# Performance work log

Measured on AMD Instinct MI355X. Metric: run time of the kernel, lower is better.

Reference implementation:

```python
import jax, jax.numpy as jnp
import numpy as np

N_NODES = 100000
N_EDGES = 3200000
IN_FEATS = 128
HIDDEN = 64
N_CLASSES = 16


def gcn_conv(x, src, dst, W, b, num_nodes):
    """PyG GCNConv (default settings): add self-loops, symmetric norm,
    linear transform, scatter-sum aggregation at dst, then bias."""
    # degree counts include self-loops (fill value 1.0)
    deg = jnp.zeros((num_nodes,), x.dtype).at[dst].add(1.0) + 1.0
    dinv = jax.lax.rsqrt(deg)  # deg >= 1, no inf handling needed
    h = x @ W  # [N, out]
    # edge messages: norm(src,dst) * h[src], aggregated at dst
    norm = dinv[src] * dinv[dst]  # [E]
    msg = h[src] * norm[:, None]  # [E, out]
    out = jax.ops.segment_sum(msg, dst, num_segments=num_nodes)
    # self-loop contribution: norm = dinv[i]^2
    out = out + h * (dinv * dinv)[:, None]
    return out + b


def setup_inputs() -> dict:
    key = jax.random.key(0)
    k1, k2, k3, k4 = jax.random.split(key, 4)
    x = jax.random.normal(k1, (N_NODES, IN_FEATS), dtype=jnp.float32)
    edge_index = jax.random.randint(k2, (2, N_EDGES), 0, N_NODES, dtype=jnp.int64)
    W1 = jax.random.normal(k3, (IN_FEATS, HIDDEN), dtype=jnp.float32) * (1.0 / np.sqrt(IN_FEATS))
    b1 = jnp.zeros((HIDDEN,), jnp.float32)
    W2 = jax.random.normal(k4, (HIDDEN, N_CLASSES), dtype=jnp.float32) * (1.0 / np.sqrt(HIDDEN))
    b2 = jnp.zeros((N_CLASSES,), jnp.float32)
    return {"x": x, "edge_index": edge_index, "W1": W1, "b1": b1, "W2": W2, "b2": b2}


def reference(x, edge_index, W1, b1, W2, b2):
    src, dst = edge_index[0], edge_index[1]
    h = gcn_conv(x, src, dst, W1, b1, N_NODES)
    h = jax.nn.relu(h)  # dropout is identity in eval mode
    out = gcn_conv(h, src, dst, W2, b2, N_NODES)
    return out
```

## Files before the change

### kernel.cpp

```cpp
#include <hip/hip_runtime.h>
#include <hip/hip_fp16.h>
#include <stdint.h>

#define N_NODES   100000
#define N_HALF    50000
#define N_EDGES   3200000
#define F_IN      128
#define F_HID     64
#define F_OUT     16

typedef _Float16 h2v __attribute__((ext_vector_type(2)));
typedef _Float16 h4v __attribute__((ext_vector_type(4)));
typedef _Float16 h8v __attribute__((ext_vector_type(8)));
typedef float    f4v __attribute__((ext_vector_type(4)));

#define BSHIFT    7
#define BK        128
#define NBUCK     782
#define NBLK_P    800
#define CHUNK_E   (N_EDGES / NBLK_P)
#define PSTRIDE   4992

#define G1_TM     64
#define G1_BLOCKS ((N_NODES + G1_TM - 1) / G1_TM)

#define OFF_RS       0
#define OFF_LEN      400000
#define OFF_DINV     800000
#define OFF_GCNT     1200000
#define OFF_CSR      1203200
#define OFF_HS1      9010688
#define OFF_OUT1A    21810688
#define OFF_OUT1B    34610688
#define OFF_HS2      47410688
#define OFF_PAIRS    OFF_OUT1A

__global__ __launch_bounds__(256, 4) void k_partition(const void* __restrict__ ei,
                                                      int* __restrict__ gcnt,
                                                      unsigned* __restrict__ pairs) {
    __shared__ unsigned long long st[CHUNK_E];
    __shared__ int h[NBUCK];
    __shared__ int cur[NBUCK];
    __shared__ int is64s;
    int t = threadIdx.x;
    if (t < 64) {
        const unsigned* u = (const unsigned*)ei;
        unsigned lo = u[2 * t], hi = u[2 * t + 1];
        int bad = (hi != 0u || lo >= 100000u) ? 1 : 0;
        unsigned long long mask = __ballot(bad);
        if (t == 0) is64s = (mask == 0ull);
    }
    for (int i = t; i < NBUCK; i += 256) { h[i] = 0; }
    __syncthreads();
    int shift = 2 + is64s;
    const char* sp = (const char*)ei;
    const char* dp = sp + ((size_t)N_EDGES << shift);
#define LDS_IDX(p, e) __builtin_nontemporal_load((const unsigned*)((p) + ((size_t)(e) << shift)))
    int base = blockIdx.x * CHUNK_E;
    int i = t;
    for (; i + 768 < CHUNK_E; i += 1024) {
        int e0 = base + i, e1 = e0 + 256, e2 = e0 + 512, e3 = e0 + 768;
        unsigned s0 = LDS_IDX(sp, e0), s1 = LDS_IDX(sp, e1);
        unsigned s2 = LDS_IDX(sp, e2), s3 = LDS_IDX(sp, e3);
        unsigned d0 = LDS_IDX(dp, e0), d1 = LDS_IDX(dp, e1);
        unsigned d2 = LDS_IDX(dp, e2), d3 = LDS_IDX(dp, e3);
        st[i]       = ((unsigned long long)s0 << 32) | d0;
        st[i + 256] = ((unsigned long long)s1 << 32) | d1;
        st[i + 512] = ((unsigned long long)s2 << 32) | d2;
        st[i + 768] = ((unsigned long long)s3 << 32) | d3;
        atomicAdd(&h[d0 >> BSHIFT], 1);
        atomicAdd(&h[d1 >> BSHIFT], 1);
        atomicAdd(&h[d2 >> BSHIFT], 1);
        atomicAdd(&h[d3 >> BSHIFT], 1);
    }
    for (; i < CHUNK_E; i += 256) {
        unsigned s = LDS_IDX(sp, base + i);
        unsigned d = LDS_IDX(dp, base + i);
        st[i] = ((unsigned long long)s << 32) | d;
        atomicAdd(&h[d >> BSHIFT], 1);
    }
#undef LDS_IDX
    __syncthreads();
    for (int j = t; j < NBUCK; j += 256) {
        int c = h[j];
        cur[j] = c ? atomicAdd(&gcnt[j], c) : 0;
    }
    __syncthreads();
    i = t;
    for (; i + 768 < CHUNK_E; i += 1024) {
        unsigned long long v0 = st[i],       v1 = st[i + 256];
        unsigned long long v2 = st[i + 512], v3 = st[i + 768];
        unsigned d0 = (unsigned)v0, d1 = (unsigned)v1;
        unsigned d2 = (unsigned)v2, d3 = (unsigned)v3;
        int p0 = atomicAdd(&cur[d0 >> BSHIFT], 1);
        int p1 = atomicAdd(&cur[d1 >> BSHIFT], 1);
        int p2 = atomicAdd(&cur[d2 >> BSHIFT], 1);
        int p3 = atomicAdd(&cur[d3 >> BSHIFT], 1);
        if (p0 < PSTRIDE) pairs[(d0 >> BSHIFT) * PSTRIDE + p0] = ((unsigned)(v0 >> 32) << BSHIFT) | (d0 & (BK - 1u));
        if (p1 < PSTRIDE) pairs[(d1 >> BSHIFT) * PSTRIDE + p1] = ((unsigned)(v1 >> 32) << BSHIFT) | (d1 & (BK - 1u));
        if (p2 < PSTRIDE) pairs[(d2 >> BSHIFT) * PSTRIDE + p2] = ((unsigned)(v2 >> 32) << BSHIFT) | (d2 & (BK - 1u));
        if (p3 < PSTRIDE) pairs[(d3 >> BSHIFT) * PSTRIDE + p3] = ((unsigned)(v3 >> 32) << BSHIFT) | (d3 & (BK - 1u));
    }
    for (; i < CHUNK_E; i += 256) {
        unsigned long long v = st[i];
        unsigned d = (unsigned)v;
        int b = d >> BSHIFT;
        int p = atomicAdd(&cur[b], 1);
        if (p < PSTRIDE)
            pairs[b * PSTRIDE + p] = ((unsigned)(v >> 32) << BSHIFT) | (d & (BK - 1u));
    }
}

__global__ __launch_bounds__(512) void k_build(const unsigned* __restrict__ pairs,
                                               const int* __restrict__ gcnt,
                                               int* __restrict__ rowstart,
                                               int* __restrict__ lens,
                                               float* __restrict__ dinv,
                                               unsigned short* __restrict__ csr) {
    __shared__ unsigned prS[PSTRIDE];
    __shared__ unsigned short csrS[PSTRIDE];
    __shared__ int c0S[BK], c1S[BK], scanS[BK], pos0[BK], pos1[BK];
    __shared__ int totpadS;
    int b = blockIdx.x, t = threadIdx.x;
    if (t < BK) { c0S[t] = 0; c1S[t] = 0; }
    __syncthreads();
    int tot = gcnt[b]; if (tot > PSTRIDE) tot = PSTRIDE;
    int base = b * PSTRIDE;
    for (int i = t; i < tot; i += 512) {
        unsigned pr = __builtin_nontemporal_load(pairs + base + i);
        prS[i] = pr;
        if ((pr >> BSHIFT) < (unsigned)N_HALF) atomicAdd(&c0S[pr & (BK - 1u)], 1);
        else                                   atomicAdd(&c1S[pr & (BK - 1u)], 1);
    }
    __syncthreads();
    int tpad = 0, p0a = 0;
    if (t < BK) {
        p0a = (c0S[t] + 3) & ~3;
        tpad = p0a + ((c1S[t] + 3) & ~3);
        scanS[t] = tpad;
    }
    __syncthreads();
    for (int off = 1; off < BK; off <<= 1) {
        int add = 0;
        if (t < BK && t >= off) add = scanS[t - off];
        __syncthreads();
        if (t < BK) scanS[t] += add;
        __syncthreads();
    }
    if (t < BK) {
        int rs = scanS[t] - tpad;
        pos0[t] = rs;
        pos1[t] = rs + p0a;
        int d = (b << BSHIFT) + t;
        if (d < N_NODES) {
            rowstart[d] = base + rs;
            lens[d] = c0S[t] | (c1S[t] << 16);
            dinv[d] = rsqrtf((float)(c0S[t] + c1S[t]) + 1.0f);
        }
        if (t == BK - 1) totpadS = scanS[BK - 1];
    }
    __syncthreads();
    for (int i = t; i < tot; i += 512) {
        unsigned pr = prS[i];
        unsigned s = pr >> BSHIFT;
        int d = pr & (BK - 1u);
        if (s < (unsigned)N_HALF) {
            int p = atomicAdd(&pos0[d], 1);
            csrS[p] = (unsigned short)s;
        } else {
            int p = atomicAdd(&pos1[d], 1);
            csrS[p] = (unsigned short)(s - N_HALF);
        }
    }
    __syncthreads();
    int nchunk = (totpadS + 7) >> 3;
    uint4* dst = (uint4*)(csr + base);
    const uint4* srcp = (const uint4*)csrS;
    for (int i = t; i < nchunk; i += 512) dst[i] = srcp[i];
}

__global__ __launch_bounds__(256, 4) void k_gemm1(const float* __restrict__ x,
                                                  const float* __restrict__ W1,
                                                  const float* __restrict__ dinv,
                                                  __half* __restrict__ hs1) {
    __shared__ _Float16 W1s[F_IN * F_HID];
    int t = threadIdx.x;
    for (int idx = t; idx < F_IN * F_HID; idx += 256) {
        int k = idx >> 6, n = idx & 63;
        float v = W1[idx];
        int kc = k >> 5, ko = (k >> 3) & 3, j = k & 7;
        int nt = n >> 4, c = n & 15;
        W1s[((kc * 4 + ko) * 4 + nt) * 128 + c * 8 + j] = (_Float16)v;
    }
    __syncthreads();
    int w = t >> 6, l = t & 63;
    int lm = l & 15, lk = l >> 4;
    int nblock = blockIdx.x * G1_TM;
    int anode = nblock + w * 16 + lm;
    int anodec = anode < N_NODES ? anode : N_NODES - 1;
    f4v acc[4] = {};
    const h8v* Bp = (const h8v*)W1s;
#pragma unroll
    for (int kc = 0; kc < 4; ++kc) {
        const f4v* src = (const f4v*)(x + (size_t)anodec * F_IN + kc * 32 + lk * 8);
        f4v v0 = __builtin_nontemporal_load(src);
        f4v v1 = __builtin_nontemporal_load(src + 1);
        h8v a;
#pragma unroll
        for (int i = 0; i < 4; ++i) {
            a[i]     = (_Float16)v0[i];
            a[i + 4] = (_Float16)v1[i];
        }
#pragma unroll
        for (int nt = 0; nt < 4; ++nt) {
            h8v b = Bp[((kc * 4 + lk) * 4 + nt) * 16 + lm];
            acc[nt] = __builtin_amdgcn_mfma_f32_16x16x32_f16(a, b, acc[nt], 0, 0, 0);
        }
    }
#pragma unroll
    for (int r = 0; r < 4; ++r) {
        int node = nblock + w * 16 + lk * 4 + r;
        if (node < N_NODES) {
            float dv = dinv[node];
#pragma unroll
            for (int nt = 0; nt < 4; ++nt) {
                float val = acc[nt][r] * dv;
                hs1[((size_t)(nt >> 1) * N_NODES + node) * 32 + (nt & 1) * 16 + lm] =
                    __float2half(val);
            }
        }
    }
}

__global__ __launch_bounds__(256) void k_agg1(const __half* __restrict__ hs1,
                                              const unsigned short* __restrict__ csr,
                                              const int* __restrict__ rowstart,
                                              const int* __restrict__ lens,
                                              __half* __restrict__ out1a,
                                              __half* __restrict__ out1b) {
    int bid = blockIdx.x;
    int combo = bid & 3;
    int chunk = combo & 1, half = combo >> 1;
    int nb = bid >> 2;
    int w = threadIdx.x >> 6, lane = threadIdx.x & 63;
    int slot = lane >> 3, fp = lane & 7;
    int n = nb * 32 + w * 8 + slot;
    const char* T = (const char*)hs1
                  + (size_t)chunk * ((size_t)N_NODES * 64)
                  + (size_t)half * ((size_t)N_HALF * 64);
    unsigned fo = fp * 8u;
    int rs = rowstart[n];
    int L = lens[n];
    int c0 = L & 0xffff;
    int start = half ? (rs + ((c0 + 3) & ~3)) : rs;
    int c = half ? (L >> 16) : c0;
    h4v a0 = {(_Float16)0.f, (_Float16)0.f, (_Float16)0.f, (_Float16)0.f};
    h4v a1 = a0, a2 = a0, a3 = a0;
    const unsigned long long* Q = (const unsigned long long*)csr;
    int q0 = start >> 2;
    int nq = c >> 2;
#define ROW1(idx) (*(const h4v*)(T + (unsigned)(idx) * 64u + fo))
    int q = 0;
    unsigned long long ea = 0ull, eb = 0ull;
    if (q + 2 <= nq) { ea = Q[q0]; eb = Q[q0 + 1]; }
    while (q + 2 <= nq) {
        unsigned long long ca = ea, cb = eb;
        q += 2;
        if (q + 2 <= nq) { ea = Q[q0 + q]; eb = Q[q0 + q + 1]; }
        h4v t0 = ROW1(ca & 0xffffu);
        h4v t1 = ROW1((ca >> 16) & 0xffffu);
        h4v t2 = ROW1((ca >> 32) & 0xffffu);
        h4v t3 = ROW1(ca >> 48);
        h4v t4 = ROW1(cb & 0xffffu);
        h4v t5 = ROW1((cb >> 16) & 0xffffu);
        h4v t6 = ROW1((cb >> 32) & 0xffffu);
        h4v t7 = ROW1(cb >> 48);
        a0 += t0; a1 += t1; a2 += t2; a3 += t3;
        a0 += t4; a1 += t5; a2 += t6; a3 += t7;
    }
    if (q < nq) {
        unsigned long long e = Q[q0 + q];
        a0 += ROW1(e & 0xffffu);
        a1 += ROW1((e >> 16) & 0xffffu);
        a2 += ROW1((e >> 32) & 0xffffu);
        a3 += ROW1(e >> 48);
    }
    for (int j = start + (nq << 2); j < start + c; ++j)
        a0 += ROW1(csr[j]);
    if ((n >= N_HALF) == (half != 0))
        a1 += ROW1(n - half * N_HALF);
#undef ROW1
    float s0 = ((float)a0[0] + (float)a1[0]) + ((float)a2[0] + (float)a3[0]);
    float s1 = ((float)a0[1] + (float)a1[1]) + ((float)a2[1] + (float)a3[1]);
    float s2 = ((float)a0[2] + (float)a1[2]) + ((float)a2[2] + (float)a3[2]);
    float s3 = ((float)a0[3] + (float)a1[3]) + ((float)a2[3] + (float)a3[3]);
    union { __half2 h[2]; float2 f; } u;
    u.h[0] = __floats2half2_rn(s0, s1);
    u.h[1] = __floats2half2_rn(s2, s3);
    __half* dst = (half ? out1b : out1a) + (size_t)n * F_HID + chunk * 32 + fp * 4;
    *(float2*)dst = u.f;
}

__global__ __launch_bounds__(256) void k_gemm2(const __half* __restrict__ out1a,
                                               const __half* __restrict__ out1b,
                                               const float* __restrict__ W2,
                                               const float* __restrict__ dinv,
                                               const float* __restrict__ b1,
                                               __half* __restrict__ hs2) {
    __shared__ float ws[F_HID * F_OUT];
    __shared__ float b1s[F_HID];
    int t = threadIdx.x;
    ((float4*)ws)[t] = ((const float4*)W2)[t];
    if (t < 16) ((float4*)b1s)[t] = ((const float4*)b1)[t];
    __syncthreads();
    int tid = blockIdx.x * 256 + t;
    int n = tid >> 2;
    if (n >= N_NODES) return;
    int cq = (tid & 3) << 2;
    float dv = dinv[n];
    const h2v* A = (const h2v*)(out1a + (size_t)n * F_HID);
    const h2v* B = (const h2v*)(out1b + (size_t)n * F_HID);
    float4 acc = make_float4(0.f, 0.f, 0.f, 0.f);
#pragma unroll 4
    for (int k4 = 0; k4 < 16; ++k4) {
        h2v pa0 = A[k4 * 2], pa1 = A[k4 * 2 + 1];
        h2v pb0 = B[k4 * 2], pb1 = B[k4 * 2 + 1];
        float h0 = fmaxf(dv * ((float)pa0.x + (float)pb0.x) + b1s[k4 * 4 + 0], 0.f);
        float h1 = fmaxf(dv * ((float)pa0.y + (float)pb0.y) + b1s[k4 * 4 + 1], 0.f);
        float h2 = fmaxf(dv * ((float)pa1.x + (float)pb1.x) + b1s[k4 * 4 + 2], 0.f);
        float h3 = fmaxf(dv * ((float)pa1.y + (float)pb1.y) + b1s[k4 * 4 + 3], 0.f);
        float4 w0 = *(const float4*)(ws + (k4 * 4 + 0) * F_OUT + cq);
        float4 w1 = *(const float4*)(ws + (k4 * 4 + 1) * F_OUT + cq);
        float4 w2 = *(const float4*)(ws + (k4 * 4 + 2) * F_OUT + cq);
        float4 w3 = *(const float4*)(ws + (k4 * 4 + 3) * F_OUT + cq);
        acc.x += h0 * w0.x + h1 * w1.x + h2 * w2.x + h3 * w3.x;
        acc.y += h0 * w0.y + h1 * w1.y + h2 * w2.y + h3 * w3.y;
        acc.z += h0 * w0.z + h1 * w1.z + h2 * w2.z + h3 * w3.z;
        acc.w += h0 * w0.w + h1 * w1.w + h2 * w2.w + h3 * w3.w;
    }
    union { __half2 h2x[2]; float2 f; } u;
    u.h2x[0] = __floats2half2_rn(acc.x * dv, acc.y * dv);
    u.h2x[1] = __floats2half2_rn(acc.z * dv, acc.w * dv);
    *(float2*)(hs2 + (size_t)n * F_OUT + cq) = u.f;
}

__global__ __launch_bounds__(128) void k_agg2(const __half* __restrict__ hs2,
                                              const unsigned short* __restrict__ csr,
                                              const int* __restrict__ rowstart,
                                              const int* __restrict__ lens,
                                              const float* __restrict__ dinv,
                                              const float* __restrict__ b2,
                                              float* __restrict__ out) {
    int w = threadIdx.x >> 6, lane = threadIdx.x & 63;
    int slot = lane >> 2, fp = lane & 3;
    int n = blockIdx.x * 32 + w * 16 + slot;
    unsigned fo = fp * 8u;
    int rs = rowstart[n];
    int L = lens[n];
    int c0 = L & 0xffff, c1 = L >> 16;
    const unsigned long long* Q = (const unsigned long long*)csr;
    h4v a0 = {(_Float16)0.f, (_Float16)0.f, (_Float16)0.f, (_Float16)0.f};
    h4v a1 = a0, a2 = a0, a3 = a0;
#pragma unroll
    for (int half = 0; half < 2; ++half) {
        const char* T = (const char*)hs2 + (size_t)half * ((size_t)N_HALF * 32);
        int start = half ? (rs + ((c0 + 3) & ~3)) : rs;
        int c = half ? c1 : c0;
        int q0 = start >> 2;
        int nq = c >> 2;
#define ROW2(idx) (*(const h4v*)(T + (unsigned)(idx) * 32u + fo))
        int q = 0;
        unsigned long long ea = 0ull, eb = 0ull;
        if (q + 2 <= nq) { ea = Q[q0]; eb = Q[q0 + 1]; }
        while (q + 2 <= nq) {
            unsigned long long ca = ea, cb = eb;
            q += 2;
            if (q + 2 <= nq) { ea = Q[q0 + q]; eb = Q[q0 + q + 1]; }
            h4v t0 = ROW2(ca & 0xffffu);
            h4v t1 = ROW2((ca >> 16) & 0xffffu);
            h4v t2 = ROW2((ca >> 32) & 0xffffu);
            h4v t3 = ROW2(ca >> 48);
            h4v t4 = ROW2(cb & 0xffffu);
            h4v t5 = ROW2((cb >> 16) & 0xffffu);
            h4v t6 = ROW2((cb >> 32) & 0xffffu);
            h4v t7 = ROW2(cb >> 48);
            a0 += t0; a1 += t1; a2 += t2; a3 += t3;
            a0 += t4; a1 += t5; a2 += t6; a3 += t7;
        }
        if (q < nq) {
            unsigned long long e = Q[q0 + q];
            a0 += ROW2(e & 0xffffu);
            a1 += ROW2((e >> 16) & 0xffffu);
            a2 += ROW2((e >> 32) & 0xffffu);
            a3 += ROW2(e >> 48);
        }
        for (int j = start + (nq << 2); j < start + c; ++j)
            a0 += ROW2(csr[j]);
#undef ROW2
    }
    a1 += *(const h4v*)((const char*)hs2 + (unsigned)n * 32u + fo);
    float dv = dinv[n];
    int fb = fp * 4;
    float s0 = ((float)a0[0] + (float)a1[0]) + ((float)a2[0] + (float)a3[0]);
    float s1 = ((float)a0[1] + (float)a1[1]) + ((float)a2[1] + (float)a3[1]);
    float s2 = ((float)a0[2] + (float)a1[2]) + ((float)a2[2] + (float)a3[2]);
    float s3 = ((float)a0[3] + (float)a1[3]) + ((float)a2[3] + (float)a3[3]);
    float ox0 = dv * s0 + b2[fb + 0];
    float ox1 = dv * s1 + b2[fb + 1];
    float ox2 = dv * s2 + b2[fb + 2];
    float ox3 = dv * s3 + b2[fb + 3];
    float4* dst = (float4*)(out + (size_t)n * F_OUT + fb);
    *dst = make_float4(ox0, ox1, ox2, ox3);
}

extern "C" void kernel_launch(void* const* d_in, const int* in_sizes, int n_in,
                              void* d_out, int out_size, void* d_ws, size_t ws_size,
                              hipStream_t stream) {
    const float* x  = (const float*)d_in[0];
    const void*  ei = d_in[1];
    const float* W1 = (const float*)d_in[2];
    const float* b1 = (const float*)d_in[3];
    const float* W2 = (const float*)d_in[4];
    const float* b2 = (const float*)d_in[5];
    float* out = (float*)d_out;

    char* ws = (char*)d_ws;
    int*            rowstart = (int*)(ws + OFF_RS);
    int*            lens     = (int*)(ws + OFF_LEN);
    float*          dinv     = (float*)(ws + OFF_DINV);
    int*            gcnt     = (int*)(ws + OFF_GCNT);
    unsigned short* csr      = (unsigned short*)(ws + OFF_CSR);
    __half*         hs1      = (__half*)(ws + OFF_HS1);
    __half*         out1a    = (__half*)(ws + OFF_OUT1A);
    __half*         out1b    = (__half*)(ws + OFF_OUT1B);
    __half*         hs2      = (__half*)(ws + OFF_HS2);
    unsigned*       pairs    = (unsigned*)(ws + OFF_PAIRS);

    (void)hipMemsetAsync(gcnt, 0, NBUCK * sizeof(int), stream);
    k_partition<<<NBLK_P, 256, 0, stream>>>(ei, gcnt, pairs);
    k_build    <<<NBUCK, 512, 0, stream>>>(pairs, gcnt, rowstart, lens, dinv, csr);

    k_gemm1<<<G1_BLOCKS, 256, 0, stream>>>(x, W1, dinv, hs1);
    k_agg1 <<<12500, 256, 0, stream>>>(hs1, csr, rowstart, lens, out1a, out1b);
    k_gemm2<<<(N_NODES * 4 + 255) / 256, 256, 0, stream>>>(out1a, out1b, W2, dinv, b1, hs2);
    k_agg2 <<<3125, 128, 0, stream>>>(hs2, csr, rowstart, lens, dinv, b2, out);
}
```

Before: 262.6 us.

## Split edge partition into histogram, offset scan and scatter kernels

Replaces the single partition kernel with three passes. A per-block bucket histogram comes first, then a per-bucket exclusive scan across blocks builds fixed write offsets, and finally a scatter pass rereads the edges and writes pairs at those offsets. This drops the large shared-memory edge staging buffer, which limited occupancy, along with the global atomic offset reservation and the host memset. The cost is a second read of the destination indices, a 5 MB count/offset matrix read with strided access, two extra launches, and no overflow guard when a bucket exceeds its stride.

```diff
diff --git a/kernel.cpp b/kernel.cpp
--- a/kernel.cpp
+++ b/kernel.cpp
@@ -17,8 +17,8 @@
 #define BSHIFT    7
 #define BK        128
 #define NBUCK     782
-#define NBLK_P    800
-#define CHUNK_E   (N_EDGES / NBLK_P)
+#define NBLK_H    1600
+#define CHUNK_H   (N_EDGES / NBLK_H)
 #define PSTRIDE   4992
 
 #define G1_TM     64
@@ -34,15 +34,11 @@
 #define OFF_OUT1B    34610688
 #define OFF_HS2      47410688
 #define OFF_PAIRS    OFF_OUT1A
-
-__global__ __launch_bounds__(256, 4) void k_partition(const void* __restrict__ ei,
-                                                      int* __restrict__ gcnt,
-                                                      unsigned* __restrict__ pairs) {
-    __shared__ unsigned long long st[CHUNK_E];
-    __shared__ int h[NBUCK];
-    __shared__ int cur[NBUCK];
+#define OFF_CNT      37425664
+#define OFF_OFFT     42430464
+
+__device__ __forceinline__ int detect_is64(const void* ei, int t) {
     __shared__ int is64s;
-    int t = threadIdx.x;
     if (t < 64) {
         const unsigned* u = (const unsigned*)ei;
         unsigned lo = u[2 * t], hi = u[2 * t + 1];
@@ -50,65 +46,112 @@
         unsigned long long mask = __ballot(bad);
         if (t == 0) is64s = (mask == 0ull);
     }
-    for (int i = t; i < NBUCK; i += 256) { h[i] = 0; }
-    __syncthreads();
-    int shift = 2 + is64s;
-    const char* sp = (const char*)ei;
-    const char* dp = sp + ((size_t)N_EDGES << shift);
-#define LDS_IDX(p, e) __builtin_nontemporal_load((const unsigned*)((p) + ((size_t)(e) << shift)))
-    int base = blockIdx.x * CHUNK_E;
+    __syncthreads();
+    return is64s;
+}
+
+__global__ __launch_bounds__(256, 4) void k_hist(const void* __restrict__ ei,
+                                                 int* __restrict__ cnt) {
+    __shared__ int h[NBUCK];
+    int t = threadIdx.x;
+    int is64 = detect_is64(ei, t);
+    for (int i = t; i < NBUCK; i += 256) h[i] = 0;
+    __syncthreads();
+    int shift = 2 + is64;
+    const char* dp = (const char*)ei + ((size_t)N_EDGES << shift);
+#define LD_IDX(p, e) __builtin_nontemporal_load((const unsigned*)((p) + ((size_t)(e) << shift)))
+    int base = blockIdx.x * CHUNK_H;
     int i = t;
-    for (; i + 768 < CHUNK_E; i += 1024) {
-        int e0 = base + i, e1 = e0 + 256, e2 = e0 + 512, e3 = e0 + 768;
-        unsigned s0 = LDS_IDX(sp, e0), s1 = LDS_IDX(sp, e1);
-        unsigned s2 = LDS_IDX(sp, e2), s3 = LDS_IDX(sp, e3);
-        unsigned d0 = LDS_IDX(dp, e0), d1 = LDS_IDX(dp, e1);
-        unsigned d2 = LDS_IDX(dp, e2), d3 = LDS_IDX(dp, e3);
-        st[i]       = ((unsigned long long)s0 << 32) | d0;
-        st[i + 256] = ((unsigned long long)s1 << 32) | d1;
-        st[i + 512] = ((unsigned long long)s2 << 32) | d2;
-        st[i + 768] = ((unsigned long long)s3 << 32) | d3;
+    for (; i + 768 < CHUNK_H; i += 1024) {
+        unsigned d0 = LD_IDX(dp, base + i);
+        unsigned d1 = LD_IDX(dp, base + i + 256);
+        unsigned d2 = LD_IDX(dp, base + i + 512);
+        unsigned d3 = LD_IDX(dp, base + i + 768);
         atomicAdd(&h[d0 >> BSHIFT], 1);
         atomicAdd(&h[d1 >> BSHIFT], 1);
         atomicAdd(&h[d2 >> BSHIFT], 1);
         atomicAdd(&h[d3 >> BSHIFT], 1);
     }
-    for (; i < CHUNK_E; i += 256) {
-        unsigned s = LDS_IDX(sp, base + i);
-        unsigned d = LDS_IDX(dp, base + i);
-        st[i] = ((unsigned long long)s << 32) | d;
+    for (; i < CHUNK_H; i += 256) {
+        unsigned d = LD_IDX(dp, base + i);
         atomicAdd(&h[d >> BSHIFT], 1);
     }
-#undef LDS_IDX
-    __syncthreads();
-    for (int j = t; j < NBUCK; j += 256) {
-        int c = h[j];
-        cur[j] = c ? atomicAdd(&gcnt[j], c) : 0;
-    }
-    __syncthreads();
-    i = t;
-    for (; i + 768 < CHUNK_E; i += 1024) {
-        unsigned long long v0 = st[i],       v1 = st[i + 256];
-        unsigned long long v2 = st[i + 512], v3 = st[i + 768];
-        unsigned d0 = (unsigned)v0, d1 = (unsigned)v1;
-        unsigned d2 = (unsigned)v2, d3 = (unsigned)v3;
+#undef LD_IDX
+    __syncthreads();
+    int* dst = cnt + (size_t)blockIdx.x * NBUCK;
+    for (int i2 = t; i2 < NBUCK; i2 += 256) dst[i2] = h[i2];
+}
+
+__global__ __launch_bounds__(256) void k_offs(const int* __restrict__ cnt,
+                                              int* __restrict__ offT,
+                                              int* __restrict__ gcnt) {
+    __shared__ int v[1792];
+    __shared__ int ts[256];
+    int b = blockIdx.x, t = threadIdx.x;
+    for (int i = t; i < 1792; i += 256)
+        v[i] = (i < NBLK_H) ? cnt[(size_t)i * NBUCK + b] : 0;
+    __syncthreads();
+    int s = 0;
+#pragma unroll
+    for (int i = 0; i < 7; ++i) s += v[t * 7 + i];
+    ts[t] = s;
+    __syncthreads();
+    for (int off = 1; off < 256; off <<= 1) {
+        int add = (t >= off) ? ts[t - off] : 0;
+        __syncthreads();
+        ts[t] += add;
+        __syncthreads();
+    }
+    int run = (t > 0) ? ts[t - 1] : 0;
+    int base = b * PSTRIDE;
+    int* od = offT + (size_t)b * NBLK_H;
+#pragma unroll
+    for (int i = 0; i < 7; ++i) {
+        int idx = t * 7 + i;
+        if (idx < NBLK_H) od[idx] = base + run;
+        run += v[t * 7 + i];
+    }
+    if (t == 255) gcnt[b] = ts[255];
+}
+
+__global__ __launch_bounds__(256, 4) void k_scatter(const void* __restrict__ ei,
+                                                    const int* __restrict__ offT,
+                                                    unsigned* __restrict__ pairs) {
+    __shared__ int cur[NBUCK];
+    int t = threadIdx.x;
+    int is64 = detect_is64(ei, t);
+    int blk = blockIdx.x;
+    for (int i = t; i < NBUCK; i += 256)
+        cur[i] = offT[(size_t)i * NBLK_H + blk];
+    __syncthreads();
+    int shift = 2 + is64;
+    const char* sp = (const char*)ei;
+    const char* dp = sp + ((size_t)N_EDGES << shift);
+#define LD_IDX(p, e) __builtin_nontemporal_load((const unsigned*)((p) + ((size_t)(e) << shift)))
+    int base = blk * CHUNK_H;
+    int i = t;
+    for (; i + 768 < CHUNK_H; i += 1024) {
+        int e0 = base + i, e1 = e0 + 256, e2 = e0 + 512, e3 = e0 + 768;
+        unsigned s0 = LD_IDX(sp, e0), s1 = LD_IDX(sp, e1);
+        unsigned s2 = LD_IDX(sp, e2), s3 = LD_IDX(sp, e3);
+        unsigned d0 = LD_IDX(dp, e0), d1 = LD_IDX(dp, e1);
+        unsigned d2 = LD_IDX(dp, e2), d3 = LD_IDX(dp, e3);
         int p0 = atomicAdd(&cur[d0 >> BSHIFT], 1);
         int p1 = atomicAdd(&cur[d1 >> BSHIFT], 1);
         int p2 = atomicAdd(&cur[d2 >> BSHIFT], 1);
         int p3 = atomicAdd(&cur[d3 >> BSHIFT], 1);
-        if (p0 < PSTRIDE) pairs[(d0 >> BSHIFT) * PSTRIDE + p0] = ((unsigned)(v0 >> 32) << BSHIFT) | (d0 & (BK - 1u));
-        if (p1 < PSTRIDE) pairs[(d1 >> BSHIFT) * PSTRIDE + p1] = ((unsigned)(v1 >> 32) << BSHIFT) | (d1 & (BK - 1u));
-        if (p2 < PSTRIDE) pairs[(d2 >> BSHIFT) * PSTRIDE + p2] = ((unsigned)(v2 >> 32) << BSHIFT) | (d2 & (BK - 1u));
-        if (p3 < PSTRIDE) pairs[(d3 >> BSHIFT) * PSTRIDE + p3] = ((unsigned)(v3 >> 32) << BSHIFT) | (d3 & (BK - 1u));
-    }
-    for (; i < CHUNK_E; i += 256) {
-        unsigned long long v = st[i];
-        unsigned d = (unsigned)v;
-        int b = d >> BSHIFT;
-        int p = atomicAdd(&cur[b], 1);
-        if (p < PSTRIDE)
-            pairs[b * PSTRIDE + p] = ((unsigned)(v >> 32) << BSHIFT) | (d & (BK - 1u));
-    }
+        pairs[p0] = (s0 << BSHIFT) | (d0 & (BK - 1u));
+        pairs[p1] = (s1 << BSHIFT) | (d1 & (BK - 1u));
+        pairs[p2] = (s2 << BSHIFT) | (d2 & (BK - 1u));
+        pairs[p3] = (s3 << BSHIFT) | (d3 & (BK - 1u));
+    }
+    for (; i < CHUNK_H; i += 256) {
+        unsigned s = LD_IDX(sp, base + i);
+        unsigned d = LD_IDX(dp, base + i);
+        int p = atomicAdd(&cur[d >> BSHIFT], 1);
+        pairs[p] = (s << BSHIFT) | (d & (BK - 1u));
+    }
+#undef LD_IDX
 }
 
 __global__ __launch_bounds__(512) void k_build(const unsigned* __restrict__ pairs,
@@ -435,10 +478,13 @@
     __half*         out1b    = (__half*)(ws + OFF_OUT1B);
     __half*         hs2      = (__half*)(ws + OFF_HS2);
     unsigned*       pairs    = (unsigned*)(ws + OFF_PAIRS);
-
-    (void)hipMemsetAsync(gcnt, 0, NBUCK * sizeof(int), stream);
-    k_partition<<<NBLK_P, 256, 0, stream>>>(ei, gcnt, pairs);
-    k_build    <<<NBUCK, 512, 0, stream>>>(pairs, gcnt, rowstart, lens, dinv, csr);
+    int*            cnt      = (int*)(ws + OFF_CNT);
+    int*            offT     = (int*)(ws + OFF_OFFT);
+
+    k_hist   <<<NBLK_H, 256, 0, stream>>>(ei, cnt);
+    k_offs   <<<NBUCK, 256, 0, stream>>>(cnt, offT, gcnt);
+    k_scatter<<<NBLK_H, 256, 0, stream>>>(ei, offT, pairs);
+    k_build  <<<NBUCK, 512, 0, stream>>>(pairs, gcnt, rowstart, lens, dinv, csr);
 
     k_gemm1<<<G1_BLOCKS, 256, 0, stream>>>(x, W1, dinv, hs1);
     k_agg1 <<<12500, 256, 0, stream>>>(hs1, csr, rowstart, lens, out1a, out1b);
```

Result: slower. 301.6 us (+14.9%).
